# Kernel optimization log

Measured on AMD Instinct MI355X. Metric: run time of the kernel, lower is better.

The kernel has to match this reference:

```python
import jax, jax.numpy as jnp
import numpy as np
import math

WIN = 8
N = WIN * WIN          # window_area = 64
H = 6                  # num_heads
DH = 32                # head_dim = dim // num_heads
DIM = 192
B_ = 8192              # batch * num_windows
LOG_MAX = math.log(1.0 / 0.01)
EPS = 1e-12            # F.normalize eps


def _checkerboard_mask():
    wm = np.ones((WIN, WIN))
    wm[0::2, 1::2] = 0
    wm[1::2, 0::2] = 0
    f = wm.reshape(-1)
    return jnp.asarray(np.outer(f, f).astype(bool))  # [N, N], True = keep


def _rel_pos_index():
    coords = np.stack(np.meshgrid(np.arange(WIN), np.arange(WIN), indexing='ij'))
    cf = coords.reshape(2, -1)
    rel = (cf[:, :, None] - cf[:, None, :]).transpose(1, 2, 0).copy()
    rel[:, :, 0] += WIN - 1
    rel[:, :, 1] += WIN - 1
    rel[:, :, 0] *= 2 * WIN - 1
    return rel.sum(-1).astype(np.int32)  # [N, N] in [0, 224]


def setup_inputs() -> dict:
    key = jax.random.key(0)
    ks = jax.random.split(key, 5)
    return {
        'x': jax.random.normal(ks[0], (B_, N, DIM), jnp.float32),
        'qkv_w': jax.random.normal(ks[1], (3 * H * DH, DIM), jnp.float32) * 0.02,
        'qkv_b': jnp.zeros((3 * H * DH,), jnp.float32),
        'proj_w': jax.random.normal(ks[2], (DIM, H * DH), jnp.float32) * 0.02,
        'proj_b': jnp.zeros((DIM,), jnp.float32),
        'logit_scale': jnp.full((H, 1, 1), math.log(10.0), jnp.float32),
        'rel_bias_table': jax.random.normal(ks[3], ((2 * WIN - 1) ** 2, H), jnp.float32) * 0.02,
        'rel_pos_index': jnp.asarray(_rel_pos_index()),
    }


def _l2norm(t):
    n = jnp.linalg.norm(t, axis=-1, keepdims=True)
    return t / jnp.maximum(n, EPS)


def reference(x, qkv_w, qkv_b, proj_w, proj_b, logit_scale, rel_bias_table, rel_pos_index):
    B = x.shape[0]
    # qkv projection -> [3, B, H, N, DH]
    qkv = (jnp.einsum('bnc,oc->bno', x, qkv_w) + qkv_b)
    qkv = qkv.reshape(B, N, 3, H, DH).transpose(2, 0, 3, 1, 4)
    q, k, v = qkv[0], qkv[1], qkv[2]

    # cosine-similarity attention logits
    attn = jnp.einsum('bhnd,bhmd->bhnm', _l2norm(q), _l2norm(k))
    scale = jnp.exp(jnp.minimum(logit_scale, LOG_MAX))  # [H,1,1]
    attn = attn * scale[None]

    # relative position bias: gather [N*N,H] -> [1,H,N,N]
    bias = rel_bias_table[rel_pos_index.reshape(-1)].reshape(N, N, H).transpose(2, 0, 1)
    attn = attn + bias[None]

    # checkerboard mask + softmax with fully-masked-row (NaN) fixup -> zeros
    cb = _checkerboard_mask()[None, None]  # [1,1,N,N]
    neg = jnp.where(cb, attn, -jnp.inf)
    m = jnp.max(neg, axis=-1, keepdims=True)
    m_safe = jnp.where(jnp.isfinite(m), m, 0.0)
    e = jnp.where(cb, jnp.exp(neg - m_safe), 0.0)
    s = jnp.sum(e, axis=-1, keepdims=True)
    p = jnp.where(s > 0, e / jnp.where(s > 0, s, 1.0), 0.0)

    out = jnp.einsum('bhnm,bhmd->bhnd', p, v)
    out = out.transpose(0, 2, 1, 3).reshape(B, N, H * DH)
    return jnp.einsum('bnd,od->bno', out, proj_w) + proj_b
```

## Files before the change

### kernel.cpp

```cpp
#include <hip/hip_runtime.h>

typedef _Float16 h8 __attribute__((ext_vector_type(8)));
typedef _Float16 h2 __attribute__((ext_vector_type(2)));
typedef float f4 __attribute__((ext_vector_type(4)));

#define NHEADS 6
#define LOGMAX 4.6051701859880914f

__device__ __forceinline__ int S_of(int j) { return ((j >> 2) << 3) + ((j & 3) << 1) + ((j >> 2) & 1); }
__device__ __forceinline__ int SC_of(int j) { return ((j >> 2) << 3) + ((j & 3) << 1) + (1 - ((j >> 2) & 1)); }

template <int CTRL>
__device__ __forceinline__ float dpp_mov(float x) {
    return __builtin_bit_cast(float,
        __builtin_amdgcn_update_dpp(0, __builtin_bit_cast(int, x), CTRL, 0xF, 0xF, true));
}
__device__ __forceinline__ float rowsum16(float x) {
    x += dpp_mov<0x121>(x);
    x += dpp_mov<0x122>(x);
    x += dpp_mov<0x124>(x);
    x += dpp_mov<0x128>(x);
    return x;
}
__device__ __forceinline__ float rowmax16(float x) {
    x = fmaxf(x, dpp_mov<0x121>(x));
    x = fmaxf(x, dpp_mov<0x122>(x));
    x = fmaxf(x, dpp_mov<0x124>(x));
    x = fmaxf(x, dpp_mov<0x128>(x));
    return x;
}
__device__ __forceinline__ unsigned pack2(float a, float b) {
    h2 v; v[0] = (_Float16)a; v[1] = (_Float16)b;
    return __builtin_bit_cast(unsigned, v);
}

__global__ void pack_kernel(const float* __restrict__ qkv_w,
                            const float* __restrict__ proj_w,
                            const float* __restrict__ rel_bias_table,
                            const int* __restrict__ rel_pos_index,
                            _Float16* __restrict__ qkvp,
                            _Float16* __restrict__ projp,
                            float* __restrict__ biask) {
    int tid = blockIdx.x * 256 + threadIdx.x;
    const int NQ = 6 * 6 * 6 * 64;
    const int NP = 6 * 12 * 64;
    if (tid < NQ) {
        int l = tid & 63;
        int rest = tid >> 6;
        int ks = rest % 6;
        int nt = (rest / 6) % 6;
        int h = rest / 36;
        int o = (nt >> 1) * 192 + h * 32 + (nt & 1) * 16 + (l & 15);
        int k0 = ks * 32 + (l >> 4) * 8;
        const float* src = qkv_w + o * 192 + k0;
        _Float16* dst = qkvp + tid * 8;
#pragma unroll
        for (int j = 0; j < 8; ++j) dst[j] = (_Float16)src[j];
    } else if (tid < NQ + NP) {
        int t = tid - NQ;
        int l = t & 63;
        int rest = t >> 6;
        int nt = rest % 12;
        int h = rest / 12;
        int o = nt * 16 + (l & 15);
        const float* srcrow = proj_w + o * 192 + h * 32;
        _Float16* dst = projp + t * 8;
        int p0 = (l >> 4) * 8;
#pragma unroll
        for (int j = 0; j < 8; ++j) {
            int p = p0 + j;
            dst[j] = (_Float16)srcrow[(p >> 1) + ((p & 1) << 4)];
        }
    } else if (tid < NQ + NP + 6 * 32 * 32) {
        int t = tid - (NQ + NP);
        int h = t >> 10;
        int jr = (t >> 5) & 31;
        int ic = t & 31;
        int rp = rel_pos_index[S_of(jr) * 64 + S_of(ic)];
        biask[t] = rel_bias_table[rp * NHEADS + h];
    }
}

__global__ __launch_bounds__(256) __attribute__((amdgpu_waves_per_eu(4, 8)))
void cwa_kernel(
    const float* __restrict__ x,
    const _Float16* __restrict__ qkvp,
    const _Float16* __restrict__ projp,
    const float* __restrict__ biask,
    const float* __restrict__ qkv_b,
    const float* __restrict__ proj_b,
    const float* __restrict__ logit_scale,
    float* __restrict__ out) {
    __shared__ __align__(16) unsigned knu[2][32][20];
    __shared__ __align__(16) _Float16 vT[2][32][40];
    __shared__ __align__(16) unsigned tmpu[4][16][20];
    __shared__ __align__(16) unsigned outSu[64][100];

    const int tid = threadIdx.x;
    const int lane = tid & 63;
    const int wave = tid >> 6;
    const int cl = lane & 15;
    const int g = lane >> 4;
    const int w0 = blockIdx.x * 2;
    const int w = wave >> 1;
    const int mh = wave & 1;

    {
        int rowi = tid >> 2;
        int sub = tid & 3;
        long base = ((long)(w0 + (rowi >> 5)) * 64 + SC_of(rowi & 31)) * 192;
#pragma unroll
        for (int i = 0; i < 12; ++i) {
            int c4 = i * 4 + sub;
            *(f4*)(out + base + c4 * 4) = *(const f4*)(proj_b + c4 * 4);
        }
    }

    h8 xf[6];
    {
        long xbase = ((long)(w0 + w) * 64 + S_of(mh * 16 + cl)) * 192;
#pragma unroll
        for (int ks = 0; ks < 6; ++ks) {
            f4 u0 = *(const f4*)(x + xbase + ks * 32 + g * 8);
            f4 u1 = *(const f4*)(x + xbase + ks * 32 + g * 8 + 4);
            h8 hv;
            hv[0] = (_Float16)u0[0]; hv[1] = (_Float16)u0[1];
            hv[2] = (_Float16)u0[2]; hv[3] = (_Float16)u0[3];
            hv[4] = (_Float16)u1[0]; hv[5] = (_Float16)u1[1];
            hv[6] = (_Float16)u1[2]; hv[7] = (_Float16)u1[3];
            xf[ks] = hv;
        }
    }

#pragma unroll 1
    for (int h = 0; h < NHEADS; ++h) {
        const _Float16* qb_h = qkvp + (long)h * 6 * 6 * 64 * 8;

        f4 acc[6];
#pragma unroll
        for (int nt = 0; nt < 6; ++nt) acc[nt] = 0.0f;
#pragma unroll
        for (int ks = 0; ks < 6; ++ks) {
#pragma unroll
            for (int nt = 0; nt < 6; ++nt) {
                h8 b = *(const h8*)(qb_h + (((nt * 6 + ks) * 64 + lane) << 3));
                acc[nt] = __builtin_amdgcn_mfma_f32_16x16x32_f16(xf[ks], b, acc[nt], 0, 0, 0);
            }
        }
        float bq0 = qkv_b[h * 32 + cl], bq1 = qkv_b[h * 32 + 16 + cl];
        float bk0 = qkv_b[192 + h * 32 + cl], bk1 = qkv_b[192 + h * 32 + 16 + cl];
        float bv0 = qkv_b[384 + h * 32 + cl], bv1 = qkv_b[384 + h * 32 + 16 + cl];
        unsigned qw[4], kw[4];
        float vv0[4], vv1[4];
#pragma unroll
        for (int r = 0; r < 4; ++r) {
            float t0 = acc[0][r] + bq0, t1 = acc[1][r] + bq1;
            float ss = rowsum16(t0 * t0 + t1 * t1);
            float rs = 1.0f / fmaxf(sqrtf(ss), 1e-12f);
            qw[r] = pack2(t0 * rs, t1 * rs);
            t0 = acc[2][r] + bk0; t1 = acc[3][r] + bk1;
            ss = rowsum16(t0 * t0 + t1 * t1);
            rs = 1.0f / fmaxf(sqrtf(ss), 1e-12f);
            kw[r] = pack2(t0 * rs, t1 * rs);
            vv0[r] = acc[4][r] + bv0;
            vv1[r] = acc[5][r] + bv1;
        }
        __syncthreads();
#pragma unroll
        for (int r = 0; r < 4; ++r) {
            int q = g * 4 + r;
            tmpu[wave][q][cl] = qw[r];
            knu[w][mh * 16 + q][cl] = kw[r];
            int kvpos = 2 * q + mh;
            vT[w][cl][kvpos] = (_Float16)vv0[r];
            vT[w][16 + cl][kvpos] = (_Float16)vv1[r];
        }
        __syncthreads();

        {
            h8 aq = *(const h8*)(&tmpu[wave][cl][g * 4]);
            f4 sN[2];
            sN[0] = 0.0f; sN[1] = 0.0f;
#pragma unroll
            for (int nt = 0; nt < 2; ++nt) {
                h8 bk_ = *(const h8*)(&knu[w][nt * 16 + cl][g * 4]);
                sN[nt] = __builtin_amdgcn_mfma_f32_16x16x32_f16(aq, bk_, sN[nt], 0, 0, 0);
            }
            float scale = __expf(fminf(logit_scale[h], LOGMAX));
            float lg[2][4];
#pragma unroll
            for (int nt = 0; nt < 2; ++nt)
#pragma unroll
                for (int r = 0; r < 4; ++r)
                    lg[nt][r] = sN[nt][r] * scale +
                                biask[h * 1024 + (mh * 16 + g * 4 + r) * 32 + nt * 16 + cl];
            unsigned pw[4];
#pragma unroll
            for (int r = 0; r < 4; ++r) {
                float mx = rowmax16(fmaxf(lg[0][r], lg[1][r]));
                float e0 = __expf(lg[0][r] - mx);
                float e1 = __expf(lg[1][r] - mx);
                float inv = 1.0f / rowsum16(e0 + e1);
                pw[r] = pack2(e0 * inv, e1 * inv);
            }
#pragma unroll
            for (int r = 0; r < 4; ++r)
                tmpu[wave][g * 4 + r][cl] = pw[r];
            h8 ap = *(const h8*)(&tmpu[wave][cl][g * 4]);
            f4 ov[2];
            ov[0] = 0.0f; ov[1] = 0.0f;
#pragma unroll
            for (int nt = 0; nt < 2; ++nt) {
                h8 bv_ = *(const h8*)(&vT[w][nt * 16 + cl][g * 8]);
                ov[nt] = __builtin_amdgcn_mfma_f32_16x16x32_f16(ap, bv_, ov[nt], 0, 0, 0);
            }
#pragma unroll
            for (int r = 0; r < 4; ++r)
                outSu[w * 32 + mh * 16 + g * 4 + r][h * 16 + cl] = pack2(ov[0][r], ov[1][r]);
        }
    }
    __syncthreads();

    {
        const int wm = wave >> 1;
        const int wn = wave & 1;
        const int r0 = wm * 32 + cl;
        const int r1 = wm * 32 + 16 + cl;
#pragma unroll 1
        for (int pass = 0; pass < 2; ++pass) {
            f4 pa0[3], pa1[3];
#pragma unroll
            for (int nt = 0; nt < 3; ++nt) { pa0[nt] = 0.0f; pa1[nt] = 0.0f; }
#pragma unroll
            for (int ks = 0; ks < 6; ++ks) {
                h8 a0 = *(const h8*)(&outSu[r0][ks * 16 + g * 4]);
                h8 a1 = *(const h8*)(&outSu[r1][ks * 16 + g * 4]);
#pragma unroll
                for (int nt = 0; nt < 3; ++nt) {
                    int ntg = wn * 6 + pass * 3 + nt;
                    h8 b = *(const h8*)(projp + (((ks * 12 + ntg) * 64 + lane) << 3));
                    pa0[nt] = __builtin_amdgcn_mfma_f32_16x16x32_f16(a0, b, pa0[nt], 0, 0, 0);
                    pa1[nt] = __builtin_amdgcn_mfma_f32_16x16x32_f16(a1, b, pa1[nt], 0, 0, 0);
                }
            }
#pragma unroll
            for (int m = 0; m < 2; ++m) {
                const f4* pm = m ? pa1 : pa0;
#pragma unroll
                for (int r = 0; r < 4; ++r) {
                    int rl = m * 16 + g * 4 + r;
                    long grow = (long)(w0 + wm) * 64 + S_of(rl);
                    float* po_ = out + grow * 192 + wn * 96 + pass * 48 + cl;
#pragma unroll
                    for (int nt = 0; nt < 3; ++nt)
                        po_[nt * 16] = pm[nt][r] + proj_b[wn * 96 + pass * 48 + nt * 16 + cl];
                }
            }
        }
    }
}

extern "C" void kernel_launch(void* const* d_in, const int* in_sizes, int n_in,
                              void* d_out, int out_size, void* d_ws, size_t ws_size,
                              hipStream_t stream) {
    const float* x = (const float*)d_in[0];
    const float* qkv_w = (const float*)d_in[1];
    const float* qkv_b = (const float*)d_in[2];
    const float* proj_w = (const float*)d_in[3];
    const float* proj_b = (const float*)d_in[4];
    const float* logit_scale = (const float*)d_in[5];
    const float* rel_bias_table = (const float*)d_in[6];
    const int* rel_pos_index = (const int*)d_in[7];
    float* out = (float*)d_out;

    const int B = in_sizes[0] / (64 * 192);

    _Float16* qkvp = (_Float16*)d_ws;
    _Float16* projp = qkvp + 6 * 6 * 6 * 64 * 8;
    float* biask = (float*)(projp + 6 * 12 * 64 * 8);

    pack_kernel<<<96, 256, 0, stream>>>(qkv_w, proj_w, rel_bias_table, rel_pos_index,
                                        qkvp, projp, biask);
    cwa_kernel<<<B / 2, 256, 0, stream>>>(x, qkvp, projp, biask, qkv_b, proj_b,
                                          logit_scale, out);
}
```

Before: 246.1 us.

## Process one window per 128-thread block instead of two per 256-thread block

```diff
diff --git a/kernel.cpp b/kernel.cpp
--- a/kernel.cpp
+++ b/kernel.cpp
@@ -81,7 +81,7 @@
     }
 }
 
-__global__ __launch_bounds__(256) __attribute__((amdgpu_waves_per_eu(4, 8)))
+__global__ __launch_bounds__(128) __attribute__((amdgpu_waves_per_eu(4, 8)))
 void cwa_kernel(
     const float* __restrict__ x,
     const _Float16* __restrict__ qkvp,
@@ -91,24 +91,22 @@
     const float* __restrict__ proj_b,
     const float* __restrict__ logit_scale,
     float* __restrict__ out) {
-    __shared__ __align__(16) unsigned knu[2][32][20];
-    __shared__ __align__(16) _Float16 vT[2][32][40];
-    __shared__ __align__(16) unsigned tmpu[4][16][20];
-    __shared__ __align__(16) unsigned outSu[64][100];
+    __shared__ __align__(16) unsigned knu[32][20];
+    __shared__ __align__(16) _Float16 vT[32][40];
+    __shared__ __align__(16) unsigned tmpu[2][16][20];
+    __shared__ __align__(16) unsigned outSu[32][100];
 
     const int tid = threadIdx.x;
     const int lane = tid & 63;
-    const int wave = tid >> 6;
+    const int mh = tid >> 6;
     const int cl = lane & 15;
     const int g = lane >> 4;
-    const int w0 = blockIdx.x * 2;
-    const int w = wave >> 1;
-    const int mh = wave & 1;
+    const long w0 = blockIdx.x;
 
     {
         int rowi = tid >> 2;
         int sub = tid & 3;
-        long base = ((long)(w0 + (rowi >> 5)) * 64 + SC_of(rowi & 31)) * 192;
+        long base = (w0 * 64 + SC_of(rowi)) * 192;
 #pragma unroll
         for (int i = 0; i < 12; ++i) {
             int c4 = i * 4 + sub;
@@ -118,7 +116,7 @@
 
     h8 xf[6];
     {
-        long xbase = ((long)(w0 + w) * 64 + S_of(mh * 16 + cl)) * 192;
+        long xbase = (w0 * 64 + S_of(mh * 16 + cl)) * 192;
 #pragma unroll
         for (int ks = 0; ks < 6; ++ks) {
             f4 u0 = *(const f4*)(x + xbase + ks * 32 + g * 8);
@@ -169,21 +167,21 @@
 #pragma unroll
         for (int r = 0; r < 4; ++r) {
             int q = g * 4 + r;
-            tmpu[wave][q][cl] = qw[r];
-            knu[w][mh * 16 + q][cl] = kw[r];
+            tmpu[mh][q][cl] = qw[r];
+            knu[mh * 16 + q][cl] = kw[r];
             int kvpos = 2 * q + mh;
-            vT[w][cl][kvpos] = (_Float16)vv0[r];
-            vT[w][16 + cl][kvpos] = (_Float16)vv1[r];
+            vT[cl][kvpos] = (_Float16)vv0[r];
+            vT[16 + cl][kvpos] = (_Float16)vv1[r];
         }
         __syncthreads();
 
         {
-            h8 aq = *(const h8*)(&tmpu[wave][cl][g * 4]);
+            h8 aq = *(const h8*)(&tmpu[mh][cl][g * 4]);
             f4 sN[2];
             sN[0] = 0.0f; sN[1] = 0.0f;
 #pragma unroll
             for (int nt = 0; nt < 2; ++nt) {
-                h8 bk_ = *(const h8*)(&knu[w][nt * 16 + cl][g * 4]);
+                h8 bk_ = *(const h8*)(&knu[nt * 16 + cl][g * 4]);
                 sN[nt] = __builtin_amdgcn_mfma_f32_16x16x32_f16(aq, bk_, sN[nt], 0, 0, 0);
             }
             float scale = __expf(fminf(logit_scale[h], LOGMAX));
@@ -205,27 +203,26 @@
             }
 #pragma unroll
             for (int r = 0; r < 4; ++r)
-                tmpu[wave][g * 4 + r][cl] = pw[r];
-            h8 ap = *(const h8*)(&tmpu[wave][cl][g * 4]);
+                tmpu[mh][g * 4 + r][cl] = pw[r];
+            h8 ap = *(const h8*)(&tmpu[mh][cl][g * 4]);
             f4 ov[2];
             ov[0] = 0.0f; ov[1] = 0.0f;
 #pragma unroll
             for (int nt = 0; nt < 2; ++nt) {
-                h8 bv_ = *(const h8*)(&vT[w][nt * 16 + cl][g * 8]);
+                h8 bv_ = *(const h8*)(&vT[nt * 16 + cl][g * 8]);
                 ov[nt] = __builtin_amdgcn_mfma_f32_16x16x32_f16(ap, bv_, ov[nt], 0, 0, 0);
             }
 #pragma unroll
             for (int r = 0; r < 4; ++r)
-                outSu[w * 32 + mh * 16 + g * 4 + r][h * 16 + cl] = pack2(ov[0][r], ov[1][r]);
+                outSu[mh * 16 + g * 4 + r][h * 16 + cl] = pack2(ov[0][r], ov[1][r]);
         }
     }
     __syncthreads();
 
     {
-        const int wm = wave >> 1;
-        const int wn = wave & 1;
-        const int r0 = wm * 32 + cl;
-        const int r1 = wm * 32 + 16 + cl;
+        const int wn = mh;
+        const int r0 = cl;
+        const int r1 = 16 + cl;
 #pragma unroll 1
         for (int pass = 0; pass < 2; ++pass) {
             f4 pa0[3], pa1[3];
@@ -249,7 +246,7 @@
 #pragma unroll
                 for (int r = 0; r < 4; ++r) {
                     int rl = m * 16 + g * 4 + r;
-                    long grow = (long)(w0 + wm) * 64 + S_of(rl);
+                    long grow = w0 * 64 + S_of(rl);
                     float* po_ = out + grow * 192 + wn * 96 + pass * 48 + cl;
 #pragma unroll
                     for (int nt = 0; nt < 3; ++nt)
@@ -281,6 +278,6 @@
 
     pack_kernel<<<96, 256, 0, stream>>>(qkv_w, proj_w, rel_bias_table, rel_pos_index,
                                         qkvp, projp, biask);
-    cwa_kernel<<<B / 2, 256, 0, stream>>>(x, qkvp, projp, biask, qkv_b, proj_b,
-                                          logit_scale, out);
-}
+    cwa_kernel<<<B, 128, 0, stream>>>(x, qkvp, projp, biask, qkv_b, proj_b,
+                                      logit_scale, out);
+}
```

New measurement: 259.3 us. 5.4% more time.

## Stage QKV weights in LDS asynchronously and fuse projection into head loop

Applied to the files above, without the earlier changes.

```diff
diff --git a/kernel.cpp b/kernel.cpp
--- a/kernel.cpp
+++ b/kernel.cpp
@@ -81,7 +81,7 @@
     }
 }
 
-__global__ __launch_bounds__(256) __attribute__((amdgpu_waves_per_eu(4, 8)))
+__global__ __launch_bounds__(256) __attribute__((amdgpu_waves_per_eu(3, 8)))
 void cwa_kernel(
     const float* __restrict__ x,
     const _Float16* __restrict__ qkvp,
@@ -91,10 +91,10 @@
     const float* __restrict__ proj_b,
     const float* __restrict__ logit_scale,
     float* __restrict__ out) {
+    __shared__ __align__(16) _Float16 wbuf[6 * 6 * 64 * 8];
     __shared__ __align__(16) unsigned knu[2][32][20];
     __shared__ __align__(16) _Float16 vT[2][32][40];
     __shared__ __align__(16) unsigned tmpu[4][16][20];
-    __shared__ __align__(16) unsigned outSu[64][100];
 
     const int tid = threadIdx.x;
     const int lane = tid & 63;
@@ -104,6 +104,19 @@
     const int w0 = blockIdx.x * 2;
     const int w = wave >> 1;
     const int mh = wave & 1;
+
+    auto stage = [&](int h) {
+        const _Float16* srcb = qkvp + (long)h * (6 * 6 * 64 * 8) + (wave * 9) * 512 + lane * 8;
+        _Float16* dstb = &wbuf[(wave * 9) * 512];
+#pragma unroll
+        for (int c = 0; c < 9; ++c)
+            __builtin_amdgcn_global_load_lds(
+                (const __attribute__((address_space(1))) unsigned*)(srcb + c * 512),
+                (__attribute__((address_space(3))) unsigned*)(dstb + c * 512),
+                16, 0, 0);
+    };
+
+    stage(0);
 
     {
         int rowi = tid >> 2;
@@ -132,9 +145,14 @@
         }
     }
 
+    f4 pacc[12];
+#pragma unroll
+    for (int nt = 0; nt < 12; ++nt) pacc[nt] = 0.0f;
+
 #pragma unroll 1
     for (int h = 0; h < NHEADS; ++h) {
-        const _Float16* qb_h = qkvp + (long)h * 6 * 6 * 64 * 8;
+        asm volatile("s_waitcnt vmcnt(0)" ::: "memory");
+        __builtin_amdgcn_s_barrier();
 
         f4 acc[6];
 #pragma unroll
@@ -143,10 +161,14 @@
         for (int ks = 0; ks < 6; ++ks) {
 #pragma unroll
             for (int nt = 0; nt < 6; ++nt) {
-                h8 b = *(const h8*)(qb_h + (((nt * 6 + ks) * 64 + lane) << 3));
+                h8 b = *(const h8*)(&wbuf[((nt * 6 + ks) * 64 + lane) * 8]);
                 acc[nt] = __builtin_amdgcn_mfma_f32_16x16x32_f16(xf[ks], b, acc[nt], 0, 0, 0);
             }
         }
+        asm volatile("s_waitcnt lgkmcnt(0)" ::: "memory");
+        __builtin_amdgcn_s_barrier();
+        if (h + 1 < NHEADS) stage(h + 1);
+
         float bq0 = qkv_b[h * 32 + cl], bq1 = qkv_b[h * 32 + 16 + cl];
         float bk0 = qkv_b[192 + h * 32 + cl], bk1 = qkv_b[192 + h * 32 + 16 + cl];
         float bv0 = qkv_b[384 + h * 32 + cl], bv1 = qkv_b[384 + h * 32 + 16 + cl];
@@ -165,7 +187,6 @@
             vv0[r] = acc[4][r] + bv0;
             vv1[r] = acc[5][r] + bv1;
         }
-        __syncthreads();
 #pragma unroll
         for (int r = 0; r < 4; ++r) {
             int q = g * 4 + r;
@@ -175,7 +196,8 @@
             vT[w][cl][kvpos] = (_Float16)vv0[r];
             vT[w][16 + cl][kvpos] = (_Float16)vv1[r];
         }
-        __syncthreads();
+        asm volatile("s_waitcnt lgkmcnt(0)" ::: "memory");
+        __builtin_amdgcn_s_barrier();
 
         {
             h8 aq = *(const h8*)(&tmpu[wave][cl][g * 4]);
@@ -216,47 +238,24 @@
             }
 #pragma unroll
             for (int r = 0; r < 4; ++r)
-                outSu[w * 32 + mh * 16 + g * 4 + r][h * 16 + cl] = pack2(ov[0][r], ov[1][r]);
-        }
-    }
-    __syncthreads();
-
-    {
-        const int wm = wave >> 1;
-        const int wn = wave & 1;
-        const int r0 = wm * 32 + cl;
-        const int r1 = wm * 32 + 16 + cl;
-#pragma unroll 1
-        for (int pass = 0; pass < 2; ++pass) {
-            f4 pa0[3], pa1[3];
-#pragma unroll
-            for (int nt = 0; nt < 3; ++nt) { pa0[nt] = 0.0f; pa1[nt] = 0.0f; }
-#pragma unroll
-            for (int ks = 0; ks < 6; ++ks) {
-                h8 a0 = *(const h8*)(&outSu[r0][ks * 16 + g * 4]);
-                h8 a1 = *(const h8*)(&outSu[r1][ks * 16 + g * 4]);
-#pragma unroll
-                for (int nt = 0; nt < 3; ++nt) {
-                    int ntg = wn * 6 + pass * 3 + nt;
-                    h8 b = *(const h8*)(projp + (((ks * 12 + ntg) * 64 + lane) << 3));
-                    pa0[nt] = __builtin_amdgcn_mfma_f32_16x16x32_f16(a0, b, pa0[nt], 0, 0, 0);
-                    pa1[nt] = __builtin_amdgcn_mfma_f32_16x16x32_f16(a1, b, pa1[nt], 0, 0, 0);
-                }
-            }
-#pragma unroll
-            for (int m = 0; m < 2; ++m) {
-                const f4* pm = m ? pa1 : pa0;
-#pragma unroll
-                for (int r = 0; r < 4; ++r) {
-                    int rl = m * 16 + g * 4 + r;
-                    long grow = (long)(w0 + wm) * 64 + S_of(rl);
-                    float* po_ = out + grow * 192 + wn * 96 + pass * 48 + cl;
-#pragma unroll
-                    for (int nt = 0; nt < 3; ++nt)
-                        po_[nt * 16] = pm[nt][r] + proj_b[wn * 96 + pass * 48 + nt * 16 + cl];
-                }
-            }
-        }
+                tmpu[wave][g * 4 + r][cl] = pack2(ov[0][r], ov[1][r]);
+            h8 am = *(const h8*)(&tmpu[wave][cl][g * 4]);
+            const _Float16* pp_h = projp + (long)h * 12 * 64 * 8;
+#pragma unroll
+            for (int nt = 0; nt < 12; ++nt) {
+                h8 bp = *(const h8*)(pp_h + ((nt * 64 + lane) << 3));
+                pacc[nt] = __builtin_amdgcn_mfma_f32_16x16x32_f16(am, bp, pacc[nt], 0, 0, 0);
+            }
+        }
+    }
+
+#pragma unroll
+    for (int r = 0; r < 4; ++r) {
+        long grow = (long)(w0 + w) * 64 + S_of(mh * 16 + g * 4 + r);
+        float* po_ = out + grow * 192 + cl;
+#pragma unroll
+        for (int nt = 0; nt < 12; ++nt)
+            po_[nt * 16] = pacc[nt][r] + proj_b[nt * 16 + cl];
     }
 }
 
```

Result: faster. 239.8 us (-2.5%).
